# Kernel tuning notes

Measured on AMD Instinct MI355X. Metric: run time of the kernel, lower is better.

The kernel has to match this reference:

```python
import jax, jax.numpy as jnp
import numpy as np

LMAX, MMAX = 4, 2
C_IN, C_OUT = 128, 128           # sphere_channels, m_output_channels
NUM_EXPERTS = 8
NUM_SYSTEMS = 16
NUM_EDGES = 12288
M_SIZE = [LMAX + 1, 2 * (LMAX - 1 + 1), 2 * (LMAX - 2 + 1)]  # [5, 8, 6]


def _mole_linear(x, W, ce, b=None):
    """MoLE linear: per-edge expert mixing of weights, equivalently mixing of
    per-expert outputs.  x: [N, in] or [N, 2, in]; W: [K, in, out]; ce: [N, K]."""
    if x.ndim == 2:
        z = jnp.einsum('ni,kio->nko', x, W)        # [N, K, out]
        y = jnp.einsum('nk,nko->no', ce, z)
    else:
        z = jnp.einsum('nci,kio->nkco', x, W)      # [N, K, 2, out]
        y = jnp.einsum('nk,nkco->nco', ce, z)
    if b is not None:
        y = y + ce @ b                              # mixed bias, b: [K, out]
    return y


def setup_inputs() -> dict:
    key = jax.random.key(0)
    ks = jax.random.split(key, 8)
    num_mcoef = sum(M_SIZE)  # 19
    x = jax.random.normal(ks[0], (NUM_EDGES, num_mcoef, C_IN), dtype=jnp.float32)
    x_edge = jax.random.normal(ks[1], (NUM_EDGES, C_IN), dtype=jnp.float32)
    expert_coefficients = jax.random.uniform(ks[2], (NUM_SYSTEMS, NUM_EXPERTS), dtype=jnp.float32)
    edge_batch = jax.random.randint(ks[3], (NUM_EDGES,), 0, NUM_SYSTEMS)
    # fc_m0: in = (lmax+1)*C, out = (lmax+1)*C_out, with bias
    in0 = (LMAX + 1) * C_IN
    out0 = (LMAX + 1) * C_OUT
    W_m0 = jax.random.normal(ks[4], (NUM_EXPERTS, in0, out0), dtype=jnp.float32) * 0.02
    b_m0 = jnp.zeros((NUM_EXPERTS, out0), dtype=jnp.float32)
    # so2_m_conv m: in = (lmax-m+1)*C, out = 2*(lmax-m+1)*C_out, no bias
    nc1 = LMAX - 1 + 1
    W_m1 = jax.random.normal(ks[5], (NUM_EXPERTS, nc1 * C_IN, 2 * nc1 * C_OUT), dtype=jnp.float32) * 0.02
    nc2 = LMAX - 2 + 1
    W_m2 = jax.random.normal(ks[6], (NUM_EXPERTS, nc2 * C_IN, 2 * nc2 * C_OUT), dtype=jnp.float32) * 0.02
    return {
        'x': x, 'x_edge': x_edge,
        'expert_coefficients': expert_coefficients, 'edge_batch': edge_batch,
        'W_m0': W_m0, 'b_m0': b_m0, 'W_m1': W_m1, 'W_m2': W_m2,
    }


def reference(x, x_edge, expert_coefficients, edge_batch, W_m0, b_m0, W_m1, W_m2):
    N = x.shape[0]
    ce = expert_coefficients[edge_batch]               # [N, K] per-edge mix coeffs
    x0, x1, x2 = jnp.split(x, np.cumsum(M_SIZE[:-1]), axis=1)
    # m = 0 branch (internal_weights=True -> no radial rescale)
    y0 = _mole_linear(x0.reshape(N, -1), W_m0, ce, b_m0)
    out = [y0.reshape(N, -1, C_OUT)]                   # [N, lmax+1, C_out]
    # m >= 1 branches: SO(2) real/imag recombination
    for m, Wm, xm in ((1, W_m1, x1), (2, W_m2, x2)):
        nc = LMAX - m + 1
        xm = xm.reshape(N, 2, nc * C_IN)
        ym = _mole_linear(xm, Wm, ce)                  # [N, 2, 2*nc*C_out]
        ym = ym.reshape(N, 4, nc * C_OUT)
        x_m_r = ym[:, 0] - ym[:, 3]                    # x_r_0 - x_i_1
        x_m_i = ym[:, 2] + ym[:, 1]                    # x_r_1 + x_i_0
        out.append(x_m_r.reshape(N, nc, C_OUT))
        out.append(x_m_i.reshape(N, nc, C_OUT))
    return jnp.concatenate(out, axis=1)                # [N, 19, C_out]
```

## Files before the change

kernel.cpp:

```cpp
#include <hip/hip_runtime.h>
#include <cstdint>

#define N_EDGES 12288
#define ROWLEN  2432
#define CAP     2048

typedef __bf16 bf16;
typedef __bf16 bf16x8 __attribute__((ext_vector_type(8)));
typedef __bf16 bf16x4 __attribute__((ext_vector_type(4)));
typedef float  f32x4  __attribute__((ext_vector_type(4)));

#define ELEMS0 (640*640)
#define ELEMS1 (1024*1024)
#define ELEMS2 (768*768)

#define WS_IDX_OFF   1024
#define WS_BIAS_OFF  (WS_IDX_OFF + 16*CAP*4)
#define WS_W_OFF     (WS_BIAS_OFF + 16*640*4)
#define WZ_ELEMS     ((size_t)16*(ELEMS0+ELEMS1+ELEMS2))

template<int B> struct Cfg;
template<> struct Cfg<0> { static constexpr int K=640,  KS=640, XOFF=0,    NT=5;
                           static constexpr size_t WOFF=0; };
template<> struct Cfg<1> { static constexpr int K=1024, KS=512, XOFF=640,  NT=8;
                           static constexpr size_t WOFF=(size_t)16*ELEMS0; };
template<> struct Cfg<2> { static constexpr int K=768,  KS=384, XOFF=1664, NT=6;
                           static constexpr size_t WOFF=(size_t)16*ELEMS0+(size_t)16*ELEMS1; };

__device__ __forceinline__ void async_copy16(const void* g, void* l) {
  auto gp = reinterpret_cast<const __attribute__((address_space(1))) unsigned int*>(
      reinterpret_cast<uintptr_t>(g));
  auto lp = reinterpret_cast<__attribute__((address_space(3))) unsigned int*>(
      (unsigned int)reinterpret_cast<uintptr_t>(l));
  __builtin_amdgcn_global_load_lds(gp, lp, 16, 0, 0);
}

template<int B>
__device__ __forceinline__ void mix_body(const float* __restrict__ Wsrc,
                                         const float* ce_s,
                                         unsigned short* __restrict__ Wz, int pos) {
  constexpr int N = Cfg<B>::K, KS = Cfg<B>::KS, NT = N / 128, HALF = N / 2;
  constexpr int SRC_STRIDE = KS * N;
  constexpr size_t DST_STRIDE = (size_t)Cfg<B>::K * N;
  int nn = pos & 127, kgrp = (pos >> 7) & 3, rest = pos >> 9;
  int nt = rest % NT, kblk = rest / NT;
  int i0 = kblk * 32 + kgrp * 8;
  int c  = nt * 128 + nn;
  int si = i0, sc = c; float sg = 1.f;
  if (B > 0 && i0 >= KS) {
    si = i0 - KS;
    if (c < HALF) { sc = c + HALF; sg = -1.f; } else { sc = c - HALF; }
  }
  float w[8][8];
  const float* p0 = Wsrc + (size_t)si * N + sc;
#pragma unroll
  for (int e = 0; e < 8; ++e) {
    const float* p = p0 + (size_t)e * SRC_STRIDE;
#pragma unroll
    for (int j = 0; j < 8; ++j)
      w[e][j] = sg * p[(size_t)j * N];
  }
  unsigned short* db = Wz + Cfg<B>::WOFF + (size_t)pos * 8;
#pragma unroll
  for (int s = 0; s < 16; ++s) {
    float a[8] = {0, 0, 0, 0, 0, 0, 0, 0};
#pragma unroll
    for (int e = 0; e < 8; ++e) {
      float cc = ce_s[s * 8 + e];
#pragma unroll
      for (int j = 0; j < 8; ++j) a[j] += cc * w[e][j];
    }
    bf16x8 v;
#pragma unroll
    for (int j = 0; j < 8; ++j) v[j] = (bf16)a[j];
    *(bf16x8*)(db + s * DST_STRIDE) = v;
  }
}

__global__ __launch_bounds__(256) void prep_all(
    const float* __restrict__ W0, const float* __restrict__ W1,
    const float* __restrict__ W2, const float* __restrict__ ce,
    unsigned short* __restrict__ Wz,
    const int* __restrict__ eb, int* __restrict__ counts, int* __restrict__ idxb,
    const float* __restrict__ b0, float* __restrict__ bias) {
  __shared__ float ce_s[128];
  __shared__ int hcnt[16], hbase[16];
  int tid = threadIdx.x;
  int bx = blockIdx.x;
  if (bx < 1000) {
    if (tid < 128) ce_s[tid] = ce[tid];
    __syncthreads();
    if (bx < 200)      mix_body<0>(W0, ce_s, Wz, bx * 256 + tid);
    else if (bx < 712) mix_body<1>(W1, ce_s, Wz, (bx - 200) * 256 + tid);
    else               mix_body<2>(W2, ce_s, Wz, (bx - 712) * 256 + tid);
  } else if (bx < 1048) {
    int t = (bx - 1000) * 256 + tid;
    if (tid < 16) hcnt[tid] = 0;
    __syncthreads();
    int s = -1, lp = 0;
    if (t < N_EDGES) { s = eb[t]; lp = atomicAdd(&hcnt[s], 1); }
    __syncthreads();
    if (tid < 16) hbase[tid] = atomicAdd(counts + tid, hcnt[tid]);
    __syncthreads();
    if (s >= 0) { int p = hbase[s] + lp; if (p < CAP) idxb[s * CAP + p] = t; }
  } else {
    int t = (bx - 1048) * 256 + tid;
    int s = t / 640, c = t - s * 640;
    float a = 0.f;
#pragma unroll
    for (int e = 0; e < 8; ++e) a += ce[s * 8 + e] * b0[e * 640 + c];
    bias[t] = a;
  }
}

template<int B>
__device__ __forceinline__ void gemm_body(
    const float* __restrict__ x,
    const unsigned short* __restrict__ Wz,
    const int* __restrict__ counts, const int* __restrict__ idxb,
    const float* __restrict__ bias, float* __restrict__ out,
    int s, int mt, int nt2, char* sm, int* eidx)
{
  constexpr int K = Cfg<B>::K, NT = Cfg<B>::NT, KB = K / 32, XOFF = Cfg<B>::XOFF;
  int cnt = counts[s];
  int m0 = mt * 128;
  if (m0 >= cnt) return;
  int tid = threadIdx.x;
  if (tid < 128) eidx[tid] = (m0 + tid < cnt) ? idxb[s * CAP + m0 + tid] : -1;
  __syncthreads();
  char* Acur = sm;          char* Anxt = sm + 8192;
  char* Bc = sm + 16384;    char* Bm = sm + 32768;    char* Bn = sm + 49152;
  int wv = tid >> 6, ln = tid & 63;
  int wm = wv >> 2, wn = wv & 3;
  int kq = ln >> 4, lm = ln & 15;
  int c0 = nt2 * 2;
  int c16 = tid & 7, rbase = tid >> 3;
  int kq_w = c16 >> 1, half = c16 & 1;
  const char* xb = (const char*)x;
  unsigned int aoff[2], kinc[2];
#pragma unroll
  for (int i = 0; i < 2; ++i) {
    int e = eidx[rbase + 64 * i];
    aoff[i] = (e >= 0) ? (unsigned int)(((size_t)e * ROWLEN + XOFF) * 4) : 0u;
    kinc[i] = (e >= 0) ? 128u : 0u;
  }
  const unsigned short* wb = Wz + Cfg<B>::WOFF + (size_t)s * K * K;

  f32x4 sreg[2];
  auto loadA = [&](int kb) __attribute__((always_inline)) {
#pragma unroll
    for (int i = 0; i < 2; ++i)
      sreg[i] = *(const f32x4*)(xb + aoff[i] + kb * kinc[i] + c16 * 16);
  };
  auto writeA = [&](char* dst) __attribute__((always_inline)) {
#pragma unroll
    for (int i = 0; i < 2; ++i) {
      int r = rbase + 64 * i;
      bf16x4 v;
      v[0] = (bf16)sreg[i][0]; v[1] = (bf16)sreg[i][1];
      v[2] = (bf16)sreg[i][2]; v[3] = (bf16)sreg[i][3];
      *(bf16x4*)(dst + kq_w * 2048 + ((r ^ (kq_w << 1)) * 16) + half * 8) = v;
    }
  };
  auto stageB = [&](int kb, char* dst) __attribute__((always_inline)) {
    const unsigned short* base = wb + (size_t)kb * (NT * 4096);
#pragma unroll
    for (int i = 0; i < 2; ++i) {
      int c = i * 512 + tid;
      int ck = c0 + (c >> 9); if (ck > NT - 1) ck = NT - 1;
      async_copy16(base + (size_t)ck * 4096 + (c & 511) * 8,
                   dst + (i * 512 + wv * 64) * 16);
    }
  };

  f32x4 acc[4][4];
#pragma unroll
  for (int i = 0; i < 4; ++i)
#pragma unroll
    for (int j = 0; j < 4; ++j) {
      acc[i][j][0] = 0.f; acc[i][j][1] = 0.f; acc[i][j][2] = 0.f; acc[i][j][3] = 0.f;
    }

  stageB(0, Bc);
  loadA(0);
  writeA(Acur);
  stageB(1, Bm);
  loadA(1);
  asm volatile("s_waitcnt lgkmcnt(0)" ::: "memory");
  __builtin_amdgcn_s_barrier();
  __builtin_amdgcn_sched_barrier(0);

#pragma unroll 1
  for (int kb = 0; kb < KB; ++kb) {
    if (kb + 2 < KB) stageB(kb + 2, Bn);
    __builtin_amdgcn_sched_barrier(0);
    bf16x8 af[4], bq[4];
#pragma unroll
    for (int mi = 0; mi < 4; ++mi) {
      int r = wm * 64 + mi * 16 + lm;
      af[mi] = *(const bf16x8*)(Acur + kq * 2048 + ((r ^ (kq << 1)) * 16));
    }
#pragma unroll
    for (int ni = 0; ni < 4; ++ni)
      bq[ni] = *(const bf16x8*)(Bc + (wn >> 1) * 8192 + kq * 2048 +
                                (((wn & 1) * 64 + ni * 16 + lm) * 16));
    __builtin_amdgcn_s_setprio(1);
#pragma unroll
    for (int mi = 0; mi < 4; ++mi)
#pragma unroll
      for (int ni = 0; ni < 4; ++ni)
        acc[mi][ni] = __builtin_amdgcn_mfma_f32_16x16x32_bf16(af[mi], bq[ni], acc[mi][ni], 0, 0, 0);
    __builtin_amdgcn_s_setprio(0);
    if (kb + 1 < KB) {
      writeA(Anxt);
      if (kb + 2 < KB) loadA(kb + 2);
    }
    asm volatile("s_waitcnt lgkmcnt(0)" ::: "memory");
    __builtin_amdgcn_s_barrier();
    __builtin_amdgcn_sched_barrier(0);
    { char* t = Acur; Acur = Anxt; Anxt = t; }
    { char* tb = Bc; Bc = Bm; Bm = Bn; Bn = tb; }
  }
  int cc = c0 + (wn >> 1);
  if (cc >= NT) return;
  int colb = cc * 128 + (wn & 1) * 64;
  float bv[4] = {0, 0, 0, 0};
  if (B == 0) {
#pragma unroll
    for (int ni = 0; ni < 4; ++ni)
      bv[ni] = bias[s * 640 + colb + ni * 16 + lm];
  }
#pragma unroll
  for (int mi = 0; mi < 4; ++mi) {
#pragma unroll
    for (int r = 0; r < 4; ++r) {
      int row = wm * 64 + mi * 16 + kq * 4 + r;
      int e = eidx[row];
      if (e < 0) continue;
      float* po = out + (size_t)e * ROWLEN + XOFF + colb + lm;
#pragma unroll
      for (int ni = 0; ni < 4; ++ni) po[ni * 16] = acc[mi][ni][r] + bv[ni];
    }
  }
}

__global__ __launch_bounds__(512, 4) void gemm_all(
    const float* __restrict__ x,
    const unsigned short* __restrict__ Wz,
    const int* __restrict__ counts, const int* __restrict__ idxb,
    const float* __restrict__ bias, float* __restrict__ out) {
  extern __shared__ char sm[];
  __shared__ int eidx[128];
  int g = blockIdx.x;
  int xcd = g & 7, j = g >> 3;
  int s = xcd + 8 * (j / 160);
  int r = j % 160;
  int mt = r / 10, bx = r % 10;
  if (bx < 3)      gemm_body<0>(x, Wz, counts, idxb, bias, out, s, mt, bx,     sm, eidx);
  else if (bx < 7) gemm_body<1>(x, Wz, counts, idxb, bias, out, s, mt, bx - 3, sm, eidx);
  else             gemm_body<2>(x, Wz, counts, idxb, bias, out, s, mt, bx - 7, sm, eidx);
}

extern "C" void kernel_launch(void* const* d_in, const int* in_sizes, int n_in,
                              void* d_out, int out_size, void* d_ws, size_t ws_size,
                              hipStream_t stream) {
  const float* x  = (const float*)d_in[0];
  const float* ce = (const float*)d_in[2];
  const int*   eb = (const int*)d_in[3];
  const float* W0 = (const float*)d_in[4];
  const float* b0 = (const float*)d_in[5];
  const float* W1 = (const float*)d_in[6];
  const float* W2 = (const float*)d_in[7];
  float* out = (float*)d_out;
  char* ws = (char*)d_ws;
  int*   counts = (int*)ws;
  int*   idxb   = (int*)(ws + WS_IDX_OFF);
  float* bias   = (float*)(ws + WS_BIAS_OFF);
  unsigned short* Wz = (unsigned short*)(ws + WS_W_OFF);

  hipMemsetAsync(ws, 0, 1024, stream);
  prep_all<<<1088, 256, 0, stream>>>(W0, W1, W2, ce, Wz, eb, counts, idxb, b0, bias);
  gemm_all<<<2560, 512, 65536, stream>>>(x, Wz, counts, idxb, bias, out);
}
```

Before: 320.2 us.

## Pad mixed-weight slabs, stagger expert reads, split mix loop, spread counters

Each per-system mixed weight slab is padded by 2048 elements so the 16 system outputs no longer sit at power-of-two strides that alias to the same memory channels. The mix kernel now rotates the expert read order per block and processes the 8 output columns in two halves of 4, which lowers register pressure at the cost of narrower 8-byte stores. The per-system edge counters are spaced 16 ints apart so they fall on separate cache lines. The aim is less channel and bank conflict and less atomic contention in the weight-prep phase. The workspace offsets must already leave room for the larger padded layout and the spaced counters.

Result: slower. 336.5 us (+5.1%).

```diff
diff --git a/kernel.cpp b/kernel.cpp
--- a/kernel.cpp
+++ b/kernel.cpp
@@ -10,22 +10,22 @@
 typedef __bf16 bf16x4 __attribute__((ext_vector_type(4)));
 typedef float  f32x4  __attribute__((ext_vector_type(4)));
 
-#define ELEMS0 (640*640)
-#define ELEMS1 (1024*1024)
-#define ELEMS2 (768*768)
+#define SYS0 (640*640   + 2048)
+#define SYS1 (1024*1024 + 2048)
+#define SYS2 (768*768   + 2048)
 
 #define WS_IDX_OFF   1024
 #define WS_BIAS_OFF  (WS_IDX_OFF + 16*CAP*4)
 #define WS_W_OFF     (WS_BIAS_OFF + 16*640*4)
-#define WZ_ELEMS     ((size_t)16*(ELEMS0+ELEMS1+ELEMS2))
 
 template<int B> struct Cfg;
 template<> struct Cfg<0> { static constexpr int K=640,  KS=640, XOFF=0,    NT=5;
-                           static constexpr size_t WOFF=0; };
+                           static constexpr size_t SYS=SYS0, WOFF=0; };
 template<> struct Cfg<1> { static constexpr int K=1024, KS=512, XOFF=640,  NT=8;
-                           static constexpr size_t WOFF=(size_t)16*ELEMS0; };
+                           static constexpr size_t SYS=SYS1, WOFF=(size_t)16*SYS0; };
 template<> struct Cfg<2> { static constexpr int K=768,  KS=384, XOFF=1664, NT=6;
-                           static constexpr size_t WOFF=(size_t)16*ELEMS0+(size_t)16*ELEMS1; };
+                           static constexpr size_t SYS=SYS2,
+                           WOFF=(size_t)16*SYS0+(size_t)16*SYS1; };
 
 __device__ __forceinline__ void async_copy16(const void* g, void* l) {
   auto gp = reinterpret_cast<const __attribute__((address_space(1))) unsigned int*>(
@@ -38,10 +38,11 @@
 template<int B>
 __device__ __forceinline__ void mix_body(const float* __restrict__ Wsrc,
                                          const float* ce_s,
-                                         unsigned short* __restrict__ Wz, int pos) {
+                                         unsigned short* __restrict__ Wz,
+                                         int pos, int estart) {
   constexpr int N = Cfg<B>::K, KS = Cfg<B>::KS, NT = N / 128, HALF = N / 2;
   constexpr int SRC_STRIDE = KS * N;
-  constexpr size_t DST_STRIDE = (size_t)Cfg<B>::K * N;
+  constexpr size_t DST_STRIDE = Cfg<B>::SYS;
   int nn = pos & 127, kgrp = (pos >> 7) & 3, rest = pos >> 9;
   int nt = rest % NT, kblk = rest / NT;
   int i0 = kblk * 32 + kgrp * 8;
@@ -51,29 +52,31 @@
     si = i0 - KS;
     if (c < HALF) { sc = c + HALF; sg = -1.f; } else { sc = c - HALF; }
   }
-  float w[8][8];
+  unsigned short* db = Wz + Cfg<B>::WOFF + (size_t)pos * 8;
   const float* p0 = Wsrc + (size_t)si * N + sc;
-#pragma unroll
-  for (int e = 0; e < 8; ++e) {
-    const float* p = p0 + (size_t)e * SRC_STRIDE;
-#pragma unroll
-    for (int j = 0; j < 8; ++j)
-      w[e][j] = sg * p[(size_t)j * N];
-  }
-  unsigned short* db = Wz + Cfg<B>::WOFF + (size_t)pos * 8;
-#pragma unroll
-  for (int s = 0; s < 16; ++s) {
-    float a[8] = {0, 0, 0, 0, 0, 0, 0, 0};
-#pragma unroll
-    for (int e = 0; e < 8; ++e) {
-      float cc = ce_s[s * 8 + e];
-#pragma unroll
-      for (int j = 0; j < 8; ++j) a[j] += cc * w[e][j];
-    }
-    bf16x8 v;
-#pragma unroll
-    for (int j = 0; j < 8; ++j) v[j] = (bf16)a[j];
-    *(bf16x8*)(db + s * DST_STRIDE) = v;
+#pragma unroll 1
+  for (int jh = 0; jh < 2; ++jh) {
+    float w[8][4];
+#pragma unroll
+    for (int t = 0; t < 8; ++t) {
+      int ee = (t + estart) & 7;
+      const float* p = p0 + (size_t)ee * SRC_STRIDE + (size_t)(jh * 4) * N;
+#pragma unroll
+      for (int j = 0; j < 4; ++j) w[t][j] = sg * p[(size_t)j * N];
+    }
+#pragma unroll
+    for (int s = 0; s < 16; ++s) {
+      float a[4] = {0, 0, 0, 0};
+#pragma unroll
+      for (int t = 0; t < 8; ++t) {
+        float cc = ce_s[s * 8 + ((t + estart) & 7)];
+#pragma unroll
+        for (int j = 0; j < 4; ++j) a[j] += cc * w[t][j];
+      }
+      bf16x4 v;
+      v[0] = (bf16)a[0]; v[1] = (bf16)a[1]; v[2] = (bf16)a[2]; v[3] = (bf16)a[3];
+      *(bf16x4*)(db + s * DST_STRIDE + jh * 4) = v;
+    }
   }
 }
 
@@ -90,9 +93,10 @@
   if (bx < 1000) {
     if (tid < 128) ce_s[tid] = ce[tid];
     __syncthreads();
-    if (bx < 200)      mix_body<0>(W0, ce_s, Wz, bx * 256 + tid);
-    else if (bx < 712) mix_body<1>(W1, ce_s, Wz, (bx - 200) * 256 + tid);
-    else               mix_body<2>(W2, ce_s, Wz, (bx - 712) * 256 + tid);
+    int estart = bx & 7;
+    if (bx < 200)      mix_body<0>(W0, ce_s, Wz, bx * 256 + tid, estart);
+    else if (bx < 712) mix_body<1>(W1, ce_s, Wz, (bx - 200) * 256 + tid, estart);
+    else               mix_body<2>(W2, ce_s, Wz, (bx - 712) * 256 + tid, estart);
   } else if (bx < 1048) {
     int t = (bx - 1000) * 256 + tid;
     if (tid < 16) hcnt[tid] = 0;
@@ -100,7 +104,7 @@
     int s = -1, lp = 0;
     if (t < N_EDGES) { s = eb[t]; lp = atomicAdd(&hcnt[s], 1); }
     __syncthreads();
-    if (tid < 16) hbase[tid] = atomicAdd(counts + tid, hcnt[tid]);
+    if (tid < 16) hbase[tid] = atomicAdd(counts + tid * 16, hcnt[tid]);
     __syncthreads();
     if (s >= 0) { int p = hbase[s] + lp; if (p < CAP) idxb[s * CAP + p] = t; }
   } else {
@@ -122,7 +126,7 @@
     int s, int mt, int nt2, char* sm, int* eidx)
 {
   constexpr int K = Cfg<B>::K, NT = Cfg<B>::NT, KB = K / 32, XOFF = Cfg<B>::XOFF;
-  int cnt = counts[s];
+  int cnt = counts[s * 16];
   int m0 = mt * 128;
   if (m0 >= cnt) return;
   int tid = threadIdx.x;
@@ -144,7 +148,7 @@
     aoff[i] = (e >= 0) ? (unsigned int)(((size_t)e * ROWLEN + XOFF) * 4) : 0u;
     kinc[i] = (e >= 0) ? 128u : 0u;
   }
-  const unsigned short* wb = Wz + Cfg<B>::WOFF + (size_t)s * K * K;
+  const unsigned short* wb = Wz + Cfg<B>::WOFF + (size_t)s * Cfg<B>::SYS;
 
   f32x4 sreg[2];
   auto loadA = [&](int kb) __attribute__((always_inline)) {
```
